# Optimization experiments

Measured on AMD Instinct MI355X. Metric: run time of the kernel, lower is better.

The kernel has to match this reference:

```python
import jax, jax.numpy as jnp
import numpy as np

TIME_STEP = 15
INIT_STATE = 0.01  # torch.full((B,H), 0.01)


def setup_inputs() -> dict:
    key = jax.random.key(0)
    k1, k2, k3, k4, k5 = jax.random.split(key, 5)
    B, IN, H = 2048, 2048, 1024
    scale_ih = 1.0 / np.sqrt(H)
    return {
        "x": jax.random.normal(k1, (B, IN), dtype=jnp.float32),
        "W_ih": jax.random.normal(k2, (4 * H, IN), dtype=jnp.float32) * scale_ih,
        "W_hh": jax.random.normal(k3, (4 * H, H), dtype=jnp.float32) * scale_ih,
        "b_ih": jax.random.normal(k4, (4 * H,), dtype=jnp.float32) * scale_ih,
        "b_hh": jax.random.normal(k5, (4 * H,), dtype=jnp.float32) * scale_ih,
    }


def reference(x, W_ih, W_hh, b_ih, b_hh):
    B = x.shape[0]
    H = W_hh.shape[1]
    # x is constant across steps -> precompute input-gate contribution once
    xg = x @ W_ih.T + b_ih  # [B, 4H]
    h0 = jnp.full((B, H), INIT_STATE, dtype=x.dtype)
    c0 = jnp.full((B, H), INIT_STATE, dtype=x.dtype)

    def step(carry, _):
        h, c = carry
        gates = xg + h @ W_hh.T + b_hh  # [B, 4H]
        i, f, g, o = jnp.split(gates, 4, axis=-1)
        i = jax.nn.sigmoid(i)
        f = jax.nn.sigmoid(f)
        g = jnp.tanh(g)
        o = jax.nn.sigmoid(o)
        c_new = f * c + i * g
        h_new = o * jnp.tanh(c_new)
        return (h_new, c_new), h_new

    _, hs = jax.lax.scan(step, (h0, c0), None, length=TIME_STEP)
    return hs  # [T, B, H]
```

## Files before the change

kernel.cpp:

```cpp
#include <hip/hip_runtime.h>
#include <hip/hip_bf16.h>

typedef float f32x4 __attribute__((ext_vector_type(4)));
typedef __bf16 bf16x8 __attribute__((ext_vector_type(8)));

#define B_SZ 2048
#define IN_SZ 2048
#define H_SZ 1024
#define G_SZ (4 * H_SZ)
#define T_STEPS 15
#define INIT_ST 0.01f

__device__ __forceinline__ float sigmoid_f(float x) { return 1.0f / (1.0f + __expf(-x)); }
__device__ __forceinline__ float tanh_f(float x)    { return 1.0f - 2.0f / (__expf(2.0f * x) + 1.0f); }

__device__ __forceinline__ void split8(f32x4 v0, f32x4 v1, bf16x8* h, bf16x8* l) {
  bf16x8 hv, lv;
  #pragma unroll
  for (int j = 0; j < 4; ++j) {
    float f = v0[j];
    __bf16 hb = (__bf16)f;
    hv[j] = hb;
    lv[j] = (__bf16)(f - (float)hb);
  }
  #pragma unroll
  for (int j = 0; j < 4; ++j) {
    float f = v1[j];
    __bf16 hb = (__bf16)f;
    hv[4 + j] = hb;
    lv[4 + j] = (__bf16)(f - (float)hb);
  }
  *h = hv;
  *l = lv;
}

__device__ __forceinline__ bf16x8 cvt8(f32x4 v0, f32x4 v1) {
  bf16x8 hv;
  #pragma unroll
  for (int j = 0; j < 4; ++j) hv[j] = (__bf16)v0[j];
  #pragma unroll
  for (int j = 0; j < 4; ++j) hv[4 + j] = (__bf16)v1[j];
  return hv;
}

__device__ __forceinline__ void gl16(const bf16x8* src, bf16x8* lds_base_uniform) {
  __builtin_amdgcn_global_load_lds(
      (const __attribute__((address_space(1))) void*)src,
      (__attribute__((address_space(3))) void*)lds_base_uniform, 16, 0, 0);
}

__global__ __launch_bounds__(256)
void repack_whh(const float* __restrict__ Whh, bf16x8* __restrict__ Wh)
{
  int cid = blockIdx.x * 256 + threadIdx.x;
  int s    = cid & 1023;
  int rest = cid >> 10;
  int ks   = rest & 31;
  int nt   = rest >> 5;
  int row  = s >> 2;
  int kc   = (s & 3) ^ (row & 3);
  int gate = row >> 6, col = row & 63;
  const float* src = Whh + (size_t)(gate * H_SZ + nt * 64 + col) * H_SZ + ks * 32 + kc * 8;
  Wh[cid] = cvt8(*(const f32x4*)src, *(const f32x4*)(src + 4));
}

__global__ __launch_bounds__(256)
void init_h0(bf16x8* __restrict__ hh, bf16x8* __restrict__ hl)
{
  int cid = blockIdx.x * 256 + threadIdx.x;
  __bf16 hi = (__bf16)INIT_ST;
  __bf16 lo = (__bf16)(INIT_ST - (float)hi);
  bf16x8 h, l;
  #pragma unroll
  for (int j = 0; j < 8; ++j) { h[j] = hi; l[j] = lo; }
  hh[cid] = h;
  hl[cid] = l;
}

__global__ __launch_bounds__(256, 2)
void xg_gemm(const float* __restrict__ x, const float* __restrict__ Wih,
             const float* __restrict__ bih, const float* __restrict__ bhh,
             float* __restrict__ xg)
{
  __shared__ bf16x8 Ah[128 * 4], Al[128 * 4], Bh[128 * 4], Bl[128 * 4];
  const int tid  = threadIdx.x;
  const int lane = tid & 63;
  const int wv   = tid >> 6;
  const int wm   = wv >> 1, wn = wv & 1;
  const int bm   = blockIdx.y * 128;
  const int bn   = blockIdx.x * 128;

  f32x4 acc[4][4] = {};

  for (int k0 = 0; k0 < IN_SZ; k0 += 32) {
    #pragma unroll
    for (int c = 0; c < 2; ++c) {
      int cid = tid + c * 256;
      int row = cid >> 2, kc = cid & 3;
      int idx = row * 4 + (kc ^ (row & 3));
      const float* srcA = x + (size_t)(bm + row) * IN_SZ + k0 + kc * 8;
      split8(*(const f32x4*)srcA, *(const f32x4*)(srcA + 4), &Ah[idx], &Al[idx]);
      const float* srcB = Wih + (size_t)(bn + row) * IN_SZ + k0 + kc * 8;
      split8(*(const f32x4*)srcB, *(const f32x4*)(srcB + 4), &Bh[idx], &Bl[idx]);
    }
    __syncthreads();

    const int kc = lane >> 4;
    bf16x8 ah[4], al[4], bh[4], bl[4];
    #pragma unroll
    for (int i = 0; i < 4; ++i) {
      int ra = wm * 64 + i * 16 + (lane & 15);
      int ia = ra * 4 + (kc ^ (ra & 3));
      ah[i] = Ah[ia]; al[i] = Al[ia];
      int rb = wn * 64 + i * 16 + (lane & 15);
      int ib = rb * 4 + (kc ^ (rb & 3));
      bh[i] = Bh[ib]; bl[i] = Bl[ib];
    }
    #pragma unroll
    for (int i = 0; i < 4; ++i)
      #pragma unroll
      for (int j = 0; j < 4; ++j) {
        acc[i][j] = __builtin_amdgcn_mfma_f32_16x16x32_bf16(ah[i], bh[j], acc[i][j], 0, 0, 0);
        acc[i][j] = __builtin_amdgcn_mfma_f32_16x16x32_bf16(ah[i], bl[j], acc[i][j], 0, 0, 0);
        acc[i][j] = __builtin_amdgcn_mfma_f32_16x16x32_bf16(al[i], bh[j], acc[i][j], 0, 0, 0);
      }
    __syncthreads();
  }

  #pragma unroll
  for (int i = 0; i < 4; ++i) {
    int m0 = bm + wm * 64 + i * 16 + ((lane >> 4) * 4);
    #pragma unroll
    for (int j = 0; j < 4; ++j) {
      int n = bn + wn * 64 + j * 16 + (lane & 15);
      float bb = bih[n] + bhh[n];
      #pragma unroll
      for (int r = 0; r < 4; ++r)
        xg[(size_t)(m0 + r) * G_SZ + n] = acc[i][j][r] + bb;
    }
  }
}

__global__ __launch_bounds__(512, 2)
void lstm_step(const bf16x8* __restrict__ hsh,
               const bf16x8* __restrict__ hsl,
               const bf16x8* __restrict__ Wh,
               const float* __restrict__ xg,
               float* __restrict__ cst,
               float* __restrict__ hout,
               bf16x8* __restrict__ hnh,
               bf16x8* __restrict__ hnl,
               int first)
{
  __shared__ __attribute__((aligned(16))) char smem[98304];
  bf16x8* AhL = (bf16x8*)smem;
  bf16x8* AlL = AhL + 3 * 512;
  bf16x8* BhL = AlL + 3 * 512;

  const int tid  = threadIdx.x;
  const int lane = tid & 63;
  const int wv   = tid >> 6;
  const int wm   = wv >> 2;
  const int wg   = wv & 3;

  const int bid  = blockIdx.x;
  const int wgid = (bid & 7) * 32 + (bid >> 3);
  const int nt   = wgid >> 4;
  const int mt   = wgid & 15;

  f32x4 acc[4][4] = {};
  const size_t abase = (size_t)mt * 32;
  const size_t bbase = (size_t)nt * 32;
  const int kc = lane >> 4;

#define STAGE(BUF, KS)                                                      \
  do {                                                                      \
    const bf16x8* sa_h = hsh + (abase + (KS)) * 512 + wv * 64 + lane;       \
    const bf16x8* sa_l = hsl + (abase + (KS)) * 512 + wv * 64 + lane;       \
    gl16(sa_h, AhL + (BUF) * 512 + wv * 64);                                \
    gl16(sa_l, AlL + (BUF) * 512 + wv * 64);                                \
    const bf16x8* sb_h = Wh + (bbase + (KS)) * 1024 + wv * 128;             \
    gl16(sb_h + lane,      BhL + (BUF) * 1024 + wv * 128);                  \
    gl16(sb_h + 64 + lane, BhL + (BUF) * 1024 + wv * 128 + 64);             \
  } while (0)

#define COMPUTE(BUF)                                                        \
  do {                                                                      \
    bf16x8 ah[4], al[4], bh[4];                                             \
    _Pragma("unroll")                                                       \
    for (int i = 0; i < 4; ++i) {                                           \
      int ra = wm * 64 + i * 16 + (lane & 15);                              \
      int ia = (BUF) * 512 + ra * 4 + (kc ^ (ra & 3));                      \
      ah[i] = AhL[ia]; al[i] = AlL[ia];                                     \
      int rb = wg * 64 + i * 16 + (lane & 15);                              \
      int ib = (BUF) * 1024 + rb * 4 + (kc ^ (rb & 3));                     \
      bh[i] = BhL[ib];                                                      \
    }                                                                       \
    __builtin_amdgcn_s_setprio(1);                                          \
    _Pragma("unroll")                                                       \
    for (int i = 0; i < 4; ++i)                                             \
      _Pragma("unroll")                                                     \
      for (int j = 0; j < 4; ++j) {                                         \
        acc[i][j] = __builtin_amdgcn_mfma_f32_16x16x32_bf16(ah[i], bh[j], acc[i][j], 0, 0, 0); \
        acc[i][j] = __builtin_amdgcn_mfma_f32_16x16x32_bf16(al[i], bh[j], acc[i][j], 0, 0, 0); \
      }                                                                     \
    __builtin_amdgcn_s_setprio(0);                                          \
  } while (0)

#define KSTEP(CUR, TGT, KST)                                                \
  do {                                                                      \
    asm volatile("s_waitcnt vmcnt(4)" ::: "memory");                        \
    __builtin_amdgcn_s_barrier();                                           \
    STAGE(TGT, KST);                                                        \
    COMPUTE(CUR);                                                           \
  } while (0)

  STAGE(0, 0);
  STAGE(1, 1);

  int ks = 0;
  #pragma unroll 1
  for (int blk = 0; blk < 10; ++blk) {
    KSTEP(0, 2, ks + 2);
    KSTEP(1, 0, ks + 3);
    KSTEP(2, 1, ks + 4);
    ks += 3;
  }
  asm volatile("s_waitcnt vmcnt(4)" ::: "memory");
  __builtin_amdgcn_s_barrier();
  COMPUTE(0);
  asm volatile("s_waitcnt vmcnt(0)" ::: "memory");
  __builtin_amdgcn_s_barrier();
  COMPUTE(1);
  __builtin_amdgcn_s_barrier();

#undef KSTEP
#undef COMPUTE
#undef STAGE

  const int bm = mt * 128, bn = nt * 64;
  const int nl = (tid & 15) * 4;
  const int ml = (tid >> 4) * 4;

  f32x4 xgv[4][4], cv[4];
  #pragma unroll
  for (int r = 0; r < 4; ++r) {
    int m = bm + ml + r;
    const float* xr = xg + (size_t)m * G_SZ + bn + nl;
    #pragma unroll
    for (int g = 0; g < 4; ++g) xgv[g][r] = *(const f32x4*)(xr + g * H_SZ);
    if (first) cv[r] = (f32x4){INIT_ST, INIT_ST, INIT_ST, INIT_ST};
    else       cv[r] = *(const f32x4*)(cst + (size_t)m * H_SZ + bn + nl);
  }

  float* pre = (float*)smem;

  if (wg < 2) {
    #pragma unroll
    for (int i = 0; i < 4; ++i)
      #pragma unroll
      for (int j = 0; j < 4; ++j) {
        int n = j * 16 + (lane & 15);
        #pragma unroll
        for (int r = 0; r < 4; ++r) {
          int m = wm * 64 + i * 16 + ((lane >> 4) * 4) + r;
          pre[(wg * 128 + m) * 68 + n] = acc[i][j][r];
        }
      }
  }
  asm volatile("s_waitcnt lgkmcnt(0)" ::: "memory");
  __builtin_amdgcn_s_barrier();

  f32x4 iv[4], fv[4];
  #pragma unroll
  for (int r = 0; r < 4; ++r) {
    int m = ml + r;
    f32x4 pi = *(const f32x4*)&pre[(0 * 128 + m) * 68 + nl];
    f32x4 pf = *(const f32x4*)&pre[(1 * 128 + m) * 68 + nl];
    #pragma unroll
    for (int j = 0; j < 4; ++j) {
      iv[r][j] = sigmoid_f(pi[j] + xgv[0][r][j]);
      fv[r][j] = sigmoid_f(pf[j] + xgv[1][r][j]);
    }
  }
  __builtin_amdgcn_s_barrier();

  if (wg >= 2) {
    #pragma unroll
    for (int i = 0; i < 4; ++i)
      #pragma unroll
      for (int j = 0; j < 4; ++j) {
        int n = j * 16 + (lane & 15);
        #pragma unroll
        for (int r = 0; r < 4; ++r) {
          int m = wm * 64 + i * 16 + ((lane >> 4) * 4) + r;
          pre[((wg - 2) * 128 + m) * 68 + n] = acc[i][j][r];
        }
      }
  }
  asm volatile("s_waitcnt lgkmcnt(0)" ::: "memory");
  __builtin_amdgcn_s_barrier();

  __bf16* ph = (__bf16*)hnh;
  __bf16* pl = (__bf16*)hnl;
  #pragma unroll
  for (int r = 0; r < 4; ++r) {
    int m = ml + r;
    f32x4 pg = *(const f32x4*)&pre[(0 * 128 + m) * 68 + nl];
    f32x4 po = *(const f32x4*)&pre[(1 * 128 + m) * 68 + nl];
    f32x4 cnew, hv;
    #pragma unroll
    for (int j = 0; j < 4; ++j) {
      float gv = tanh_f(pg[j] + xgv[2][r][j]);
      float ov = sigmoid_f(po[j] + xgv[3][r][j]);
      cnew[j] = fv[r][j] * cv[r][j] + iv[r][j] * gv;
      hv[j]   = ov * tanh_f(cnew[j]);
    }
    int mg = bm + m;
    *(f32x4*)(cst  + (size_t)mg * H_SZ + bn + nl) = cnew;
    *(f32x4*)(hout + (size_t)mg * H_SZ + bn + nl) = hv;

    int nglob = bn + nl;
    int ks2 = nglob >> 5;
    int kc2 = (nglob >> 3) & 3;
    int eb  = nglob & 7;
    int s2  = m * 4 + (kc2 ^ (m & 3));
    size_t ci = (((size_t)mt * 32 + ks2) * 512 + s2) * 8 + eb;
    union { __bf16 b[4]; uint2 u; } uh, ul;
    #pragma unroll
    for (int j = 0; j < 4; ++j) {
      __bf16 hb = (__bf16)hv[j];
      uh.b[j] = hb;
      ul.b[j] = (__bf16)(hv[j] - (float)hb);
    }
    *(uint2*)(ph + ci) = uh.u;
    *(uint2*)(pl + ci) = ul.u;
  }
}

extern "C" void kernel_launch(void* const* d_in, const int* in_sizes, int n_in,
                              void* d_out, int out_size, void* d_ws, size_t ws_size,
                              hipStream_t stream)
{
  const float* x   = (const float*)d_in[0];
  const float* Wih = (const float*)d_in[1];
  const float* Whh = (const float*)d_in[2];
  const float* bih = (const float*)d_in[3];
  const float* bhh = (const float*)d_in[4];
  float* out = (float*)d_out;

  float*  xg  = (float*)d_ws;
  float*  cst = xg + (size_t)B_SZ * G_SZ;
  bf16x8* Wh  = (bf16x8*)(cst + (size_t)B_SZ * H_SZ);
  bf16x8* hAh = Wh + 524288;
  bf16x8* hAl = hAh + 262144;
  bf16x8* hBh = hAl + 262144;
  bf16x8* hBl = hBh + 262144;

  repack_whh<<<2048, 256, 0, stream>>>(Whh, Wh);
  init_h0<<<1024, 256, 0, stream>>>(hAh, hAl);
  xg_gemm<<<dim3(G_SZ / 128, B_SZ / 128), 256, 0, stream>>>(x, Wih, bih, bhh, xg);

  for (int t = 0; t < T_STEPS; ++t) {
    const bf16x8* rh = (t & 1) ? hBh : hAh;
    const bf16x8* rl = (t & 1) ? hBl : hAl;
    bf16x8* wh = (t & 1) ? hAh : hBh;
    bf16x8* wl = (t & 1) ? hAl : hBl;
    lstm_step<<<256, 512, 0, stream>>>(rh, rl, Wh, xg, cst,
                                       out + (size_t)t * B_SZ * H_SZ, wh, wl,
                                       t == 0 ? 1 : 0);
  }
}
```

Measured before the change: 882.1 us.

## Halve LSTM step tile rows and double-buffer LDS fragment reads in registers

Each lstm_step block now computes 64 batch rows instead of 128, using 4 waves of 256 threads, and the launch uses 512 blocks. The K loop now reads the next stage's A/B fragments from LDS into a second register set while MFMAs run on the current set, with a three-slot global-to-LDS pipeline. The h-state repack layout changes to a 256-entry stride per k-slice to match the smaller tile. The aims are to hide LDS read latency behind MFMAs and to put more blocks on the device. The cost is that each W_hh tile is reloaded by twice as many blocks, and the doubled fragment registers may reduce occupancy.

```diff
diff --git a/kernel.cpp b/kernel.cpp
--- a/kernel.cpp
+++ b/kernel.cpp
@@ -141,7 +141,7 @@
   }
 }
 
-__global__ __launch_bounds__(512, 2)
+__global__ __launch_bounds__(256, 2)
 void lstm_step(const bf16x8* __restrict__ hsh,
                const bf16x8* __restrict__ hsl,
                const bf16x8* __restrict__ Wh,
@@ -152,93 +152,115 @@
                bf16x8* __restrict__ hnl,
                int first)
 {
-  __shared__ __attribute__((aligned(16))) char smem[98304];
-  bf16x8* AhL = (bf16x8*)smem;
-  bf16x8* AlL = AhL + 3 * 512;
-  bf16x8* BhL = AlL + 3 * 512;
+  __shared__ __attribute__((aligned(16))) char smem[73728];
+  bf16x8* L = (bf16x8*)smem;
 
   const int tid  = threadIdx.x;
   const int lane = tid & 63;
   const int wv   = tid >> 6;
-  const int wm   = wv >> 2;
-  const int wg   = wv & 3;
+  const int wg   = wv;
 
   const int bid  = blockIdx.x;
-  const int wgid = (bid & 7) * 32 + (bid >> 3);
-  const int nt   = wgid >> 4;
-  const int mt   = wgid & 15;
+  const int wgid = (bid & 7) * 64 + (bid >> 3);
+  const int nt   = wgid >> 5;
+  const int mt   = wgid & 31;
 
   f32x4 acc[4][4] = {};
   const size_t abase = (size_t)mt * 32;
   const size_t bbase = (size_t)nt * 32;
   const int kc = lane >> 4;
 
+  bf16x8 ahA[4], alA[4], bhA[4];
+  bf16x8 ahB[4], alB[4], bhB[4];
+
 #define STAGE(BUF, KS)                                                      \
   do {                                                                      \
-    const bf16x8* sa_h = hsh + (abase + (KS)) * 512 + wv * 64 + lane;       \
-    const bf16x8* sa_l = hsl + (abase + (KS)) * 512 + wv * 64 + lane;       \
-    gl16(sa_h, AhL + (BUF) * 512 + wv * 64);                                \
-    gl16(sa_l, AlL + (BUF) * 512 + wv * 64);                                \
-    const bf16x8* sb_h = Wh + (bbase + (KS)) * 1024 + wv * 128;             \
-    gl16(sb_h + lane,      BhL + (BUF) * 1024 + wv * 128);                  \
-    gl16(sb_h + 64 + lane, BhL + (BUF) * 1024 + wv * 128 + 64);             \
+    gl16(hsh + (abase + (KS)) * 256 + tid, L + (BUF) * 1536 + wv * 64);     \
+    gl16(hsl + (abase + (KS)) * 256 + tid, L + (BUF) * 1536 + 256 + wv * 64); \
+    const bf16x8* sb = Wh + (bbase + (KS)) * 1024;                          \
+    gl16(sb + tid,       L + (BUF) * 1536 + 512 + wv * 64);                 \
+    gl16(sb + 256 + tid, L + (BUF) * 1536 + 768 + wv * 64);                 \
+    gl16(sb + 512 + tid, L + (BUF) * 1536 + 1024 + wv * 64);                \
+    gl16(sb + 768 + tid, L + (BUF) * 1536 + 1280 + wv * 64);                \
   } while (0)
 
-#define COMPUTE(BUF)                                                        \
+#define READF(S, BUF)                                                       \
   do {                                                                      \
-    bf16x8 ah[4], al[4], bh[4];                                             \
     _Pragma("unroll")                                                       \
     for (int i = 0; i < 4; ++i) {                                           \
-      int ra = wm * 64 + i * 16 + (lane & 15);                              \
-      int ia = (BUF) * 512 + ra * 4 + (kc ^ (ra & 3));                      \
-      ah[i] = AhL[ia]; al[i] = AlL[ia];                                     \
+      int ra = i * 16 + (lane & 15);                                        \
+      int ca = (BUF) * 1536 + ra * 4 + (kc ^ (ra & 3));                     \
+      ah##S[i] = L[ca];                                                     \
+      al##S[i] = L[ca + 256];                                               \
       int rb = wg * 64 + i * 16 + (lane & 15);                              \
-      int ib = (BUF) * 1024 + rb * 4 + (kc ^ (rb & 3));                     \
-      bh[i] = BhL[ib];                                                      \
+      int cb = (BUF) * 1536 + 512 + rb * 4 + (kc ^ (rb & 3));               \
+      bh##S[i] = L[cb];                                                     \
     }                                                                       \
+  } while (0)
+
+#define MFMAF(S)                                                            \
+  do {                                                                      \
     __builtin_amdgcn_s_setprio(1);                                          \
     _Pragma("unroll")                                                       \
     for (int i = 0; i < 4; ++i)                                             \
       _Pragma("unroll")                                                     \
       for (int j = 0; j < 4; ++j) {                                         \
-        acc[i][j] = __builtin_amdgcn_mfma_f32_16x16x32_bf16(ah[i], bh[j], acc[i][j], 0, 0, 0); \
-        acc[i][j] = __builtin_amdgcn_mfma_f32_16x16x32_bf16(al[i], bh[j], acc[i][j], 0, 0, 0); \
+        acc[i][j] = __builtin_amdgcn_mfma_f32_16x16x32_bf16(ah##S[i], bh##S[j], acc[i][j], 0, 0, 0); \
+        acc[i][j] = __builtin_amdgcn_mfma_f32_16x16x32_bf16(al##S[i], bh##S[j], acc[i][j], 0, 0, 0); \
       }                                                                     \
     __builtin_amdgcn_s_setprio(0);                                          \
   } while (0)
 
-#define KSTEP(CUR, TGT, KST)                                                \
+#define ITER(KS, SB, RB, RS, MS)                                            \
   do {                                                                      \
-    asm volatile("s_waitcnt vmcnt(4)" ::: "memory");                        \
+    asm volatile("s_waitcnt lgkmcnt(0)" ::: "memory");                      \
+    asm volatile("s_waitcnt vmcnt(6)" ::: "memory");                        \
     __builtin_amdgcn_s_barrier();                                           \
-    STAGE(TGT, KST);                                                        \
-    COMPUTE(CUR);                                                           \
+    STAGE(SB, (KS) + 3);                                                    \
+    READF(RS, RB);                                                          \
+    MFMAF(MS);                                                              \
   } while (0)
 
   STAGE(0, 0);
   STAGE(1, 1);
-
-  int ks = 0;
+  STAGE(2, 2);
+  asm volatile("s_waitcnt vmcnt(12)" ::: "memory");
+  __builtin_amdgcn_s_barrier();
+  READF(A, 0);
+
   #pragma unroll 1
-  for (int blk = 0; blk < 10; ++blk) {
-    KSTEP(0, 2, ks + 2);
-    KSTEP(1, 0, ks + 3);
-    KSTEP(2, 1, ks + 4);
-    ks += 3;
-  }
-  asm volatile("s_waitcnt vmcnt(4)" ::: "memory");
-  __builtin_amdgcn_s_barrier();
-  COMPUTE(0);
+  for (int r6 = 0; r6 < 24; r6 += 6) {
+    ITER(r6 + 0, 0, 1, B, A);
+    ITER(r6 + 1, 1, 2, A, B);
+    ITER(r6 + 2, 2, 0, B, A);
+    ITER(r6 + 3, 0, 1, A, B);
+    ITER(r6 + 4, 1, 2, B, A);
+    ITER(r6 + 5, 2, 0, A, B);
+  }
+  ITER(24, 0, 1, B, A);
+  ITER(25, 1, 2, A, B);
+  ITER(26, 2, 0, B, A);
+  ITER(27, 0, 1, A, B);
+  ITER(28, 1, 2, B, A);
+  asm volatile("s_waitcnt lgkmcnt(0)" ::: "memory");
+  asm volatile("s_waitcnt vmcnt(6)" ::: "memory");
+  __builtin_amdgcn_s_barrier();
+  READF(A, 0);
+  MFMAF(B);
+  asm volatile("s_waitcnt lgkmcnt(0)" ::: "memory");
   asm volatile("s_waitcnt vmcnt(0)" ::: "memory");
   __builtin_amdgcn_s_barrier();
-  COMPUTE(1);
-  __builtin_amdgcn_s_barrier();
-
-#undef KSTEP
-#undef COMPUTE
+  READF(B, 1);
+  MFMAF(A);
+  MFMAF(B);
+  __builtin_amdgcn_s_barrier();
+
+#undef ITER
+#undef MFMAF
+#undef READF
 #undef STAGE
 
-  const int bm = mt * 128, bn = nt * 64;
+  const int bm = mt * 64, bn = nt * 64;
   const int nl = (tid & 15) * 4;
   const int ml = (tid >> 4) * 4;
 
@@ -263,8 +285,8 @@
         int n = j * 16 + (lane & 15);
         #pragma unroll
         for (int r = 0; r < 4; ++r) {
-          int m = wm * 64 + i * 16 + ((lane >> 4) * 4) + r;
-          pre[(wg * 128 + m) * 68 + n] = acc[i][j][r];
+          int m = i * 16 + ((lane >> 4) * 4) + r;
+          pre[(wg * 64 + m) * 68 + n] = acc[i][j][r];
         }
       }
   }
@@ -275,8 +297,8 @@
   #pragma unroll
   for (int r = 0; r < 4; ++r) {
     int m = ml + r;
-    f32x4 pi = *(const f32x4*)&pre[(0 * 128 + m) * 68 + nl];
-    f32x4 pf = *(const f32x4*)&pre[(1 * 128 + m) * 68 + nl];
+    f32x4 pi = *(const f32x4*)&pre[(0 * 64 + m) * 68 + nl];
+    f32x4 pf = *(const f32x4*)&pre[(1 * 64 + m) * 68 + nl];
     #pragma unroll
     for (int j = 0; j < 4; ++j) {
       iv[r][j] = sigmoid_f(pi[j] + xgv[0][r][j]);
@@ -293,8 +315,8 @@
         int n = j * 16 + (lane & 15);
         #pragma unroll
         for (int r = 0; r < 4; ++r) {
-          int m = wm * 64 + i * 16 + ((lane >> 4) * 4) + r;
-          pre[((wg - 2) * 128 + m) * 68 + n] = acc[i][j][r];
+          int m = i * 16 + ((lane >> 4) * 4) + r;
+          pre[((wg - 2) * 64 + m) * 68 + n] = acc[i][j][r];
         }
       }
   }
@@ -306,8 +328,8 @@
   #pragma unroll
   for (int r = 0; r < 4; ++r) {
     int m = ml + r;
-    f32x4 pg = *(const f32x4*)&pre[(0 * 128 + m) * 68 + nl];
-    f32x4 po = *(const f32x4*)&pre[(1 * 128 + m) * 68 + nl];
+    f32x4 pg = *(const f32x4*)&pre[(0 * 64 + m) * 68 + nl];
+    f32x4 po = *(const f32x4*)&pre[(1 * 64 + m) * 68 + nl];
     f32x4 cnew, hv;
     #pragma unroll
     for (int j = 0; j < 4; ++j) {
@@ -325,7 +347,7 @@
     int kc2 = (nglob >> 3) & 3;
     int eb  = nglob & 7;
     int s2  = m * 4 + (kc2 ^ (m & 3));
-    size_t ci = (((size_t)mt * 32 + ks2) * 512 + s2) * 8 + eb;
+    size_t ci = (((size_t)mt * 32 + ks2) * 256 + s2) * 8 + eb;
     union { __bf16 b[4]; uint2 u; } uh, ul;
     #pragma unroll
     for (int j = 0; j < 4; ++j) {
@@ -366,7 +388,7 @@
     const bf16x8* rl = (t & 1) ? hBl : hAl;
     bf16x8* wh = (t & 1) ? hAh : hBh;
     bf16x8* wl = (t & 1) ? hAl : hBl;
-    lstm_step<<<256, 512, 0, stream>>>(rh, rl, Wh, xg, cst,
+    lstm_step<<<512, 256, 0, stream>>>(rh, rl, Wh, xg, cst,
                                        out + (size_t)t * B_SZ * H_SZ, wh, wl,
                                        t == 0 ? 1 : 0);
   }
```

Result: no change. 869.4 us (-1.4%).
